# Kernel tuning notes

Measured on AMD Instinct MI355X. Metric: run time of the kernel, lower is better.

## Reference

```python
import jax, jax.numpy as jnp
import numpy as np

DIM = 256
NUM_HEADS = 8
HEAD_DIM = DIM // NUM_HEADS


def _conv1x1(x, W, scale, bias):
    # 1x1 conv (bias=False) + eval-mode BN folded to per-channel scale/shift
    y = jnp.einsum('oc,bchw->bohw', W, x)
    return y * scale[None, :, None, None] + bias[None, :, None, None]


def setup_inputs() -> dict:
    key = jax.random.key(0)
    ks = jax.random.split(key, 16)
    B, H, W = 4, 64, 64
    Hu, Wu = 32, 32
    inp = {
        'x': jax.random.normal(ks[0], (B, DIM, H, W), jnp.float32),
        'upper_feat': jax.random.normal(ks[1], (B, DIM, Hu, Wu), jnp.float32),
        'Wq': jax.random.normal(ks[2], (DIM, DIM), jnp.float32) * 0.02,
        'q_scale': jax.random.uniform(ks[3], (DIM,), jnp.float32, 0.5, 1.5),
        'q_bias': jax.random.normal(ks[4], (DIM,), jnp.float32) * 0.02,
        'Wkv': jax.random.normal(ks[5], (2 * DIM, DIM), jnp.float32) * 0.02,
        'kv_scale': jax.random.uniform(ks[6], (2 * DIM,), jnp.float32, 0.5, 1.5),
        'kv_bias': jax.random.normal(ks[7], (2 * DIM,), jnp.float32) * 0.02,
        'Wpe': jax.random.normal(ks[8], (DIM, 1, 7, 7), jnp.float32) * 0.02,
        'pe_scale': jax.random.uniform(ks[9], (DIM,), jnp.float32, 0.5, 1.5),
        'pe_bias': jax.random.normal(ks[10], (DIM,), jnp.float32) * 0.02,
        'Wproj': jax.random.normal(ks[11], (DIM, DIM), jnp.float32) * 0.02,
        'proj_scale': jax.random.uniform(ks[12], (DIM,), jnp.float32, 0.5, 1.5),
        'proj_bias': jax.random.normal(ks[13], (DIM,), jnp.float32) * 0.02,
    }
    return inp


def reference(x, upper_feat, Wq, q_scale, q_bias, Wkv, kv_scale, kv_bias,
              Wpe, pe_scale, pe_bias, Wproj, proj_scale, proj_bias):
    B, C, H, W = x.shape
    N = H * W
    _, _, Hu, Wu = upper_feat.shape
    Nu = Hu * Wu

    # q branch: 1x1 conv+BN on x -> [B, heads, N, head_dim]
    q = _conv1x1(x, Wq, q_scale, q_bias)
    q = q.reshape(B, NUM_HEADS, HEAD_DIM, N).transpose(0, 1, 3, 2)

    # kv branch on upper (coarser) feature -> [B, heads, Nu, 2*head_dim]
    kv = _conv1x1(upper_feat, Wkv, kv_scale, kv_bias)
    kv = kv.reshape(B, NUM_HEADS, 2 * HEAD_DIM, Nu).transpose(0, 1, 3, 2)
    k, v = kv[..., :HEAD_DIM], kv[..., HEAD_DIM:]

    # cross attention: q over x pixels, k/v over upper pixels
    sim = jnp.einsum('bhnd,bhmd->bhnm', q, k) * (HEAD_DIM ** -0.5)
    attn = jax.nn.softmax(sim, axis=-1)
    ao = jnp.einsum('bhnm,bhmd->bhnd', attn, v)  # [B,h,N,hd]
    ao = ao.transpose(0, 1, 3, 2).reshape(B, C, H, W)

    # positional-encoding branch: depthwise 7x7 conv on v at upper resolution
    v_r = v.transpose(0, 1, 3, 2).reshape(B, C, Hu, Wu)
    v_pe = jax.lax.conv_general_dilated(
        v_r, Wpe, window_strides=(1, 1), padding=((3, 3), (3, 3)),
        feature_group_count=C,
        dimension_numbers=('NCHW', 'OIHW', 'NCHW'))
    v_pe = v_pe * pe_scale[None, :, None, None] + pe_bias[None, :, None, None]
    # bilinear upsample to x resolution (align_corners=False semantics)
    v_pe = jax.image.resize(v_pe, (B, C, H, W), method='bilinear')

    out = ao + v_pe
    return _conv1x1(out, Wproj, proj_scale, proj_bias)
```

## Files before the change

kernel.cpp:

```cpp
#include <hip/hip_runtime.h>
#include <hip/hip_bf16.h>

#define DIM 256
#define NHEADS 8
#define HDIM 32
#define Bq 4
#define Nq 4096
#define Nu 1024

typedef __attribute__((ext_vector_type(8))) short bf16x8;
typedef __attribute__((ext_vector_type(16))) float f32x16;
typedef __attribute__((ext_vector_type(4))) unsigned short us4;

__device__ __forceinline__ ushort f2bf(float x) {
    union { float f; unsigned u; } v; v.f = x;
    unsigned r = v.u + 0x7fffu + ((v.u >> 16) & 1u);
    return (ushort)(r >> 16);
}
__device__ __forceinline__ float bf2f(ushort u) {
    union { unsigned u; float f; } v; v.u = ((unsigned)u) << 16;
    return v.f;
}

__global__ __launch_bounds__(256) void prepro(
    const float* __restrict__ Wq, ushort* __restrict__ Oq,
    const float* __restrict__ Wkv, ushort* __restrict__ Okv,
    const float* __restrict__ Wp, ushort* __restrict__ Oph, ushort* __restrict__ Opl,
    const float* __restrict__ x, ushort* __restrict__ xT,
    const float* __restrict__ upper, ushort* __restrict__ upT)
{
    __shared__ ushort T[64][66];
    const int id = blockIdx.x;
    const int tid = threadIdx.x;

    if (id < 512) {
        int i = id * 256 + tid;
        if (i < 65536) {
            Oq[i] = f2bf(Wq[i]);
            float w = Wp[i];
            ushort h = f2bf(w);
            Oph[i] = h;
            Opl[i] = f2bf(w - bf2f(h));
        }
        Okv[i] = f2bf(Wkv[i]);
        return;
    }

    const float* In; ushort* OutT; int N, n0, c0, b;
    if (id < 1536) {
        int q = id - 512;
        In = x; OutT = xT; N = 4096;
        n0 = (q & 63) * 64; c0 = ((q >> 6) & 3) * 64; b = q >> 8;
    } else {
        int q = id - 1536;
        In = upper; OutT = upT; N = 1024;
        n0 = (q & 15) * 64; c0 = ((q >> 4) & 3) * 64; b = q >> 6;
    }

    const float* Ib = In + ((size_t)b * 256 + c0) * N + n0;
    const int nx = (tid & 15) * 4, cy = tid >> 4;
    #pragma unroll
    for (int p = 0; p < 4; ++p) {
        float4 v = *(const float4*)(Ib + (size_t)(cy + p * 16) * N + nx);
        T[nx + 0][cy + p * 16] = f2bf(v.x);
        T[nx + 1][cy + p * 16] = f2bf(v.y);
        T[nx + 2][cy + p * 16] = f2bf(v.z);
        T[nx + 3][cy + p * 16] = f2bf(v.w);
    }
    __syncthreads();
    ushort* Ob = OutT + ((size_t)b * N + n0) * 256 + c0;
    #pragma unroll
    for (int p = 0; p < 4; ++p) {
        int row = (tid >> 4) + p * 16;
        *(us4*)(Ob + (size_t)row * 256 + (tid & 15) * 4) = *(const us4*)&T[row][(tid & 15) * 4];
    }
}

__global__ __launch_bounds__(256, 4) void qkv_mfma(
    const ushort* __restrict__ Wqb, const ushort* __restrict__ xT,
    const float* __restrict__ q_scale, const float* __restrict__ q_bias, float qmult,
    const ushort* __restrict__ Wkvb, const ushort* __restrict__ upT,
    const float* __restrict__ kv_scale, const float* __restrict__ kv_bias,
    ushort* __restrict__ Qb, ushort* __restrict__ Kb, ushort* __restrict__ Vb)
{
    const int KD = 256;
    const int id = blockIdx.x;
    const int tid = threadIdx.x;
    const int w = tid >> 6, l = tid & 63;
    const int l31 = l & 31, hi = l >> 5;

    const ushort *Wb, *InT, *OutA; const float *scale, *bias;
    int N, n0, o0, b; float mult; bool isT; int bh;
    if (id < 512) {
        int q = id;
        int bx = q & 15, by = (q >> 4) & 7; b = q >> 7;
        N = 4096; n0 = (bx * 4 + w) * 64; o0 = by * 32;
        Wb = Wqb; InT = xT; scale = q_scale; bias = q_bias; mult = qmult;
        isT = true; bh = b * 8 + (o0 >> 5);
        OutA = Qb;
    } else {
        int q = id - 512;
        int bx = q & 3, by = (q >> 2) & 15; b = q >> 6;
        N = 1024; n0 = (bx * 4 + w) * 64; o0 = by * 32;
        Wb = Wkvb; InT = upT; scale = kv_scale; bias = kv_bias; mult = 1.0f;
        isT = ((o0 & 32) == 0); bh = b * 8 + (o0 >> 6);
        OutA = Kb;
    }

    const ushort* Wp = Wb + (size_t)(o0 + l31) * KD + hi * 8;
    const ushort* I0 = InT + ((size_t)b * N + n0 + l31) * KD + hi * 8;
    const ushort* I1 = I0 + (size_t)32 * KD;

    f32x16 acc0 = {}, acc1 = {};
    if (isT) {
        #pragma unroll 8
        for (int kk = 0; kk < KD; kk += 16) {
            bf16x8 wv = *(const bf16x8*)(Wp + kk);
            bf16x8 i0 = *(const bf16x8*)(I0 + kk);
            bf16x8 i1 = *(const bf16x8*)(I1 + kk);
            acc0 = __builtin_amdgcn_mfma_f32_32x32x16_bf16(i0, wv, acc0, 0, 0, 0);
            acc1 = __builtin_amdgcn_mfma_f32_32x32x16_bf16(i1, wv, acc1, 0, 0, 0);
        }
        const float sc = scale[o0 + l31] * mult;
        const float bi = bias[o0 + l31] * mult;
        ushort* Oa = (ushort*)OutA + ((size_t)bh * N) * 32 + l31;
        #pragma unroll
        for (int r = 0; r < 16; ++r) {
            const int dn = (r & 3) + 8 * (r >> 2) + 4 * hi;
            Oa[(size_t)(n0 + dn) * 32]      = f2bf(acc0[r] * sc + bi);
            Oa[(size_t)(n0 + 32 + dn) * 32] = f2bf(acc1[r] * sc + bi);
        }
    } else {
        #pragma unroll 8
        for (int kk = 0; kk < KD; kk += 16) {
            bf16x8 wv = *(const bf16x8*)(Wp + kk);
            bf16x8 i0 = *(const bf16x8*)(I0 + kk);
            bf16x8 i1 = *(const bf16x8*)(I1 + kk);
            acc0 = __builtin_amdgcn_mfma_f32_32x32x16_bf16(wv, i0, acc0, 0, 0, 0);
            acc1 = __builtin_amdgcn_mfma_f32_32x32x16_bf16(wv, i1, acc1, 0, 0, 0);
        }
        ushort* Ob = Vb + (size_t)bh * 32 * N;
        #pragma unroll
        for (int r = 0; r < 16; ++r) {
            const int dr = (r & 3) + 8 * (r >> 2) + 4 * hi;
            const float sc = scale[o0 + dr], bi = bias[o0 + dr];
            Ob[(size_t)dr * N + n0 + l31]      = f2bf(acc0[r] * sc + bi);
            Ob[(size_t)dr * N + n0 + 32 + l31] = f2bf(acc1[r] * sc + bi);
        }
    }
}

__global__ __launch_bounds__(256, 4) void attn_dw(
    const ushort* __restrict__ Qb, const ushort* __restrict__ Kt,
    const ushort* __restrict__ Vb, ushort* __restrict__ ao,
    const float* __restrict__ Wpe, const float* __restrict__ pe_scale,
    const float* __restrict__ pe_bias, ushort* __restrict__ vpe)
{
    __shared__ __align__(16) unsigned char smem[16384];
    const int tid = threadIdx.x;

    if (blockIdx.x < 1024) {
        const int w = tid >> 6, l = tid & 63;
        const int l31 = l & 31, hi = l >> 5;
        const int lid = blockIdx.x;
        const int j = lid >> 3;
        const int bh = (lid & 7) * 4 + (j >> 5);
        const int qbase = (j & 31) * 128 + w * 32;

        unsigned char (*ldsbuf)[8192] = (unsigned char(*)[8192])smem;

        const ushort* Qp = Qb + ((size_t)bh * 4096 + qbase) * 32;
        const unsigned char* Kg = (const unsigned char*)(Kt + (size_t)bh * 1024 * 32);
        const unsigned char* Vg = (const unsigned char*)(Vb + (size_t)bh * 32 * 1024);

        const bf16x8 qb0 = *(const bf16x8*)(Qp + (size_t)l31 * 32 + hi * 8);
        const bf16x8 qb1 = *(const bf16x8*)(Qp + (size_t)l31 * 32 + 16 + hi * 8);

        const int kr = tid >> 2, kc = tid & 3;
        const int vd = tid >> 3, vc = tid & 7;
        const int kwr = (kr * 64 + kc * 16) ^ ((kr & 7) << 4);
        const int vwr = vd * 128 + ((vc ^ (vd & 7)) << 4);

        f32x16 acc = {};
        float l_run = 0.f;

        uint4 kreg = *(const uint4*)(Kg + kr * 64 + kc * 16);
        uint4 vreg = *(const uint4*)(Vg + vd * 2048 + vc * 16);
        *(uint4*)(&ldsbuf[0][kwr]) = kreg;
        *(uint4*)(&ldsbuf[0][4096 + vwr]) = vreg;
        __syncthreads();

        for (int ph = 0; ph < 16; ++ph) {
            const int cur = ph & 1;
            if (ph < 15) {
                const size_t koff = (size_t)(ph + 1) * 4096;
                const int    voff = (ph + 1) * 128;
                kreg = *(const uint4*)(Kg + koff + kr * 64 + kc * 16);
                vreg = *(const uint4*)(Vg + (size_t)vd * 2048 + voff + vc * 16);
            }
            const unsigned char* Kl = &ldsbuf[cur][0];
            const unsigned char* Vl = &ldsbuf[cur][4096];

            #pragma unroll
            for (int s = 0; s < 2; ++s) {
                const int r = s * 32 + l31;
                bf16x8 ka0 = *(const bf16x8*)(Kl + ((r * 64 + hi * 16) ^ ((r & 7) << 4)));
                bf16x8 ka1 = *(const bf16x8*)(Kl + ((r * 64 + 32 + hi * 16) ^ ((r & 7) << 4)));
                bf16x8 va0 = *(const bf16x8*)(Vl + l31 * 128 + (((s * 4 + hi)     ^ (l31 & 7)) << 4));
                bf16x8 va1 = *(const bf16x8*)(Vl + l31 * 128 + (((s * 4 + 2 + hi) ^ (l31 & 7)) << 4));

                f32x16 sv = {};
                sv = __builtin_amdgcn_mfma_f32_32x32x16_bf16(ka0, qb0, sv, 0, 0, 0);
                sv = __builtin_amdgcn_mfma_f32_32x32x16_bf16(ka1, qb1, sv, 0, 0, 0);

                float p[16];
                #pragma unroll
                for (int r2 = 0; r2 < 16; ++r2) p[r2] = __builtin_amdgcn_exp2f(sv[r2]);
                l_run += (((p[0] + p[1]) + (p[2] + p[3])) + ((p[4] + p[5]) + (p[6] + p[7])))
                       + (((p[8] + p[9]) + (p[10] + p[11])) + ((p[12] + p[13]) + (p[14] + p[15])));

                int c[8];
                #pragma unroll
                for (int i = 0; i < 8; ++i)
                    asm("v_cvt_pk_bf16_f32 %0, %1, %2" : "=v"(c[i]) : "v"(p[2 * i]), "v"(p[2 * i + 1]));
                asm("v_permlane32_swap_b32 %0, %1" : "+v"(c[0]), "+v"(c[2]));
                asm("v_permlane32_swap_b32 %0, %1" : "+v"(c[1]), "+v"(c[3]));
                asm("v_permlane32_swap_b32 %0, %1" : "+v"(c[4]), "+v"(c[6]));
                asm("v_permlane32_swap_b32 %0, %1" : "+v"(c[5]), "+v"(c[7]));

                union { int i[4]; bf16x8 v; } b0u, b1u;
                b0u.i[0] = c[0]; b0u.i[1] = c[1]; b0u.i[2] = c[2]; b0u.i[3] = c[3];
                b1u.i[0] = c[4]; b1u.i[1] = c[5]; b1u.i[2] = c[6]; b1u.i[3] = c[7];

                acc = __builtin_amdgcn_mfma_f32_32x32x16_bf16(va0, b0u.v, acc, 0, 0, 0);
                acc = __builtin_amdgcn_mfma_f32_32x32x16_bf16(va1, b1u.v, acc, 0, 0, 0);
            }

            if (ph < 15) {
                const int nxt = cur ^ 1;
                *(uint4*)(&ldsbuf[nxt][kwr]) = kreg;
                *(uint4*)(&ldsbuf[nxt][4096 + vwr]) = vreg;
            }
            __syncthreads();
        }

        l_run += __shfl_xor(l_run, 32);
        float inv = 1.0f / l_run;

        ushort* aob = ao + ((size_t)(bh >> 3) * 256 + (bh & 7) * 32) * 4096 + qbase + l31;
        #pragma unroll
        for (int r = 0; r < 16; ++r) {
            const int d = (r & 3) + 8 * (r >> 2) + 4 * hi;
            aob[(size_t)d * 4096] = f2bf(acc[r] * inv);
        }
    } else {
        const int bc = blockIdx.x - 1024;
        const int b = bc >> 8, c = bc & 255;
        const ushort* vp = Vb + ((size_t)(b * 8 + (c >> 5)) * 32 + (c & 31)) * 1024;

        float* t   = (float*)smem;
        float* v32 = (float*)(smem + 5776);
        float* wl  = (float*)(smem + 9872);

        for (int i = tid; i < 38 * 38; i += 256) {
            int yy = i / 38 - 3, xx = i % 38 - 3;
            t[i] = (yy >= 0 && yy < 32 && xx >= 0 && xx < 32) ? bf2f(vp[yy * 32 + xx]) : 0.f;
        }
        if (tid < 49) wl[tid] = Wpe[(size_t)c * 49 + tid];
        __syncthreads();

        const float sc = pe_scale[c], bi = pe_bias[c];
        for (int i = tid; i < 1024; i += 256) {
            int y = i >> 5, x = i & 31;
            float s = 0.f;
            #pragma unroll
            for (int ky = 0; ky < 7; ++ky)
                #pragma unroll
                for (int kx = 0; kx < 7; ++kx)
                    s += t[(y + ky) * 38 + x + kx] * wl[ky * 7 + kx];
            v32[i] = s * sc + bi;
        }
        __syncthreads();

        ushort* op = vpe + (size_t)bc * 4096;
        #pragma unroll
        for (int p = 0; p < 16; ++p) {
            int idx = p * 256 + tid;
            int x = idx & 63, y = idx >> 6;
            float cx = x * 0.5f - 0.25f;
            float cy = y * 0.5f - 0.25f;
            int x0 = (x - 1) >> 1, y0 = (y - 1) >> 1;
            float fx = cx - x0, fy = cy - y0;
            int x0c = max(x0, 0), x1c = min(x0 + 1, 31);
            int y0c = max(y0, 0), y1c = min(y0 + 1, 31);
            float v00 = v32[y0c * 32 + x0c], v01 = v32[y0c * 32 + x1c];
            float v10 = v32[y1c * 32 + x0c], v11 = v32[y1c * 32 + x1c];
            float val = (1.f - fy) * ((1.f - fx) * v00 + fx * v01)
                      + fy * ((1.f - fx) * v10 + fx * v11);
            op[idx] = f2bf(val);
        }
    }
}

__global__ __launch_bounds__(256) void prep(
    const ushort* __restrict__ ao, const ushort* __restrict__ vpe,
    ushort* __restrict__ AT)
{
    __shared__ ushort T[64][66];
    const int n0 = blockIdx.x * 64, c0 = blockIdx.y * 64, b = blockIdx.z;
    const int tid = threadIdx.x;
    const ushort* ab = ao  + ((size_t)b * 256 + c0) * 4096 + n0;
    const ushort* vb = vpe + ((size_t)b * 256 + c0) * 4096 + n0;
    const int nx = (tid & 15) * 4, cy = tid >> 4;
    #pragma unroll
    for (int p = 0; p < 4; ++p) {
        const int c = cy + p * 16;
        us4 a = *(const us4*)(ab + (size_t)c * 4096 + nx);
        us4 v = *(const us4*)(vb + (size_t)c * 4096 + nx);
        T[nx + 0][c] = f2bf(bf2f(a.x) + bf2f(v.x));
        T[nx + 1][c] = f2bf(bf2f(a.y) + bf2f(v.y));
        T[nx + 2][c] = f2bf(bf2f(a.z) + bf2f(v.z));
        T[nx + 3][c] = f2bf(bf2f(a.w) + bf2f(v.w));
    }
    __syncthreads();
    ushort* Ob = AT + ((size_t)b * 4096 + n0) * 256 + c0;
    #pragma unroll
    for (int p = 0; p < 4; ++p) {
        int row = (tid >> 4) + p * 16;
        *(us4*)(Ob + (size_t)row * 256 + (tid & 15) * 4) = *(const us4*)&T[row][(tid & 15) * 4];
    }
}

__global__ __launch_bounds__(256, 2) void proj_mfma(
    const ushort* __restrict__ Whi, const ushort* __restrict__ Wlo,
    const ushort* __restrict__ A,
    const float* __restrict__ scale, const float* __restrict__ bias,
    float* __restrict__ Out)
{
    const int KD = 256;
    const int tid = threadIdx.x;
    const int w = tid >> 6, l = tid & 63;
    const int l31 = l & 31, hi = l >> 5;
    const int b = blockIdx.z;
    const int n0 = (blockIdx.x * 4 + w) * 64;
    const int o0 = blockIdx.y * 32;

    const ushort* wh  = Whi + (size_t)(o0 + l31) * KD + hi * 8;
    const ushort* wlp = Wlo + (size_t)(o0 + l31) * KD + hi * 8;
    const ushort* a0  = A + ((size_t)b * 4096 + n0 + l31) * KD + hi * 8;
    const ushort* a1  = a0 + (size_t)32 * KD;

    f32x16 acc0 = {}, acc1 = {};
    #pragma unroll 4
    for (int kk = 0; kk < KD; kk += 16) {
        bf16x8 awh = *(const bf16x8*)(wh + kk);
        bf16x8 awl = *(const bf16x8*)(wlp + kk);
        bf16x8 av0 = *(const bf16x8*)(a0 + kk);
        bf16x8 av1 = *(const bf16x8*)(a1 + kk);
        acc0 = __builtin_amdgcn_mfma_f32_32x32x16_bf16(awh, av0, acc0, 0, 0, 0);
        acc1 = __builtin_amdgcn_mfma_f32_32x32x16_bf16(awh, av1, acc1, 0, 0, 0);
        acc0 = __builtin_amdgcn_mfma_f32_32x32x16_bf16(awl, av0, acc0, 0, 0, 0);
        acc1 = __builtin_amdgcn_mfma_f32_32x32x16_bf16(awl, av1, acc1, 0, 0, 0);
    }

    float* Ob = Out + (size_t)b * 256 * 4096;
    #pragma unroll
    for (int r = 0; r < 16; ++r) {
        const int o = o0 + (r & 3) + 8 * (r >> 2) + 4 * hi;
        const float sc = scale[o], bi = bias[o];
        Ob[(size_t)o * 4096 + n0 + l31]      = acc0[r] * sc + bi;
        Ob[(size_t)o * 4096 + n0 + 32 + l31] = acc1[r] * sc + bi;
    }
}

extern "C" void kernel_launch(void* const* d_in, const int* in_sizes, int n_in,
                              void* d_out, int out_size, void* d_ws, size_t ws_size,
                              hipStream_t stream)
{
    const float* x        = (const float*)d_in[0];
    const float* upper    = (const float*)d_in[1];
    const float* Wq       = (const float*)d_in[2];
    const float* q_scale  = (const float*)d_in[3];
    const float* q_bias   = (const float*)d_in[4];
    const float* Wkv      = (const float*)d_in[5];
    const float* kv_scale = (const float*)d_in[6];
    const float* kv_bias  = (const float*)d_in[7];
    const float* Wpe      = (const float*)d_in[8];
    const float* pe_scale = (const float*)d_in[9];
    const float* pe_bias  = (const float*)d_in[10];
    const float* Wproj    = (const float*)d_in[11];
    const float* proj_scale = (const float*)d_in[12];
    const float* proj_bias  = (const float*)d_in[13];
    float* out = (float*)d_out;

    ushort* Qb   = (ushort*)d_ws;
    ushort* Kb   = Qb + (size_t)32 * 4096 * 32;
    ushort* Vb   = Kb + (size_t)32 * 1024 * 32;
    ushort* ao   = Vb + (size_t)32 * 1024 * 32;
    ushort* AT   = ao + (size_t)Bq * DIM * Nq;
    ushort* Wqb  = AT + (size_t)Bq * Nq * DIM;
    ushort* Wkvb = Wqb + 256 * 256;
    ushort* Wph  = Wkvb + 512 * 256;
    ushort* Wpl  = Wph + 256 * 256;
    ushort* xT   = ao;
    ushort* upT  = AT;
    ushort* vpe  = (ushort*)out;

    const float qmult = 0.17677669529663687f * 1.4426950408889634f;

    prepro<<<dim3(1792), 256, 0, stream>>>(Wq, Wqb, Wkv, Wkvb, Wproj, Wph, Wpl,
                                           x, xT, upper, upT);

    qkv_mfma<<<dim3(768), 256, 0, stream>>>(Wqb, xT, q_scale, q_bias, qmult,
                                            Wkvb, upT, kv_scale, kv_bias,
                                            Qb, Kb, Vb);

    attn_dw<<<dim3(2048), 256, 0, stream>>>(Qb, Kb, Vb, ao,
                                            Wpe, pe_scale, pe_bias, vpe);

    prep<<<dim3(64, 4, 4), 256, 0, stream>>>(ao, vpe, AT);

    proj_mfma<<<dim3(16, 8, 4), 256, 0, stream>>>(Wph, Wpl, AT,
                                                  proj_scale, proj_bias, out);
}
```

Measured before the change: 90.13 us.

## Fuse residual add and transpose into projection GEMM via swizzled LDS tile

Removes the separate prep kernel, which summed ao and vpe and wrote a transposed bf16 buffer. Each proj_mfma block now loads a 64-pixel by 256-channel tile of both inputs, adds them, packs to bf16 and stores it transposed into XOR-swizzled shared memory before the MFMA loop reads it. The tiling also changes: each block covers 128 output channels, which lets the staged activations be reused across more weight rows, and vpe gets its own workspace buffer instead of aliasing the output. The cost is 32KB of LDS per block, which may limit occupancy, and each of the two o-blocks per tile re-reads and re-adds the same inputs.

```diff
diff --git a/kernel.cpp b/kernel.cpp
--- a/kernel.cpp
+++ b/kernel.cpp
@@ -302,74 +302,96 @@
     }
 }
 
-__global__ __launch_bounds__(256) void prep(
-    const ushort* __restrict__ ao, const ushort* __restrict__ vpe,
-    ushort* __restrict__ AT)
-{
-    __shared__ ushort T[64][66];
-    const int n0 = blockIdx.x * 64, c0 = blockIdx.y * 64, b = blockIdx.z;
-    const int tid = threadIdx.x;
-    const ushort* ab = ao  + ((size_t)b * 256 + c0) * 4096 + n0;
-    const ushort* vb = vpe + ((size_t)b * 256 + c0) * 4096 + n0;
-    const int nx = (tid & 15) * 4, cy = tid >> 4;
-    #pragma unroll
-    for (int p = 0; p < 4; ++p) {
-        const int c = cy + p * 16;
-        us4 a = *(const us4*)(ab + (size_t)c * 4096 + nx);
-        us4 v = *(const us4*)(vb + (size_t)c * 4096 + nx);
-        T[nx + 0][c] = f2bf(bf2f(a.x) + bf2f(v.x));
-        T[nx + 1][c] = f2bf(bf2f(a.y) + bf2f(v.y));
-        T[nx + 2][c] = f2bf(bf2f(a.z) + bf2f(v.z));
-        T[nx + 3][c] = f2bf(bf2f(a.w) + bf2f(v.w));
-    }
-    __syncthreads();
-    ushort* Ob = AT + ((size_t)b * 4096 + n0) * 256 + c0;
-    #pragma unroll
-    for (int p = 0; p < 4; ++p) {
-        int row = (tid >> 4) + p * 16;
-        *(us4*)(Ob + (size_t)row * 256 + (tid & 15) * 4) = *(const us4*)&T[row][(tid & 15) * 4];
-    }
-}
-
 __global__ __launch_bounds__(256, 2) void proj_mfma(
     const ushort* __restrict__ Whi, const ushort* __restrict__ Wlo,
-    const ushort* __restrict__ A,
+    const ushort* __restrict__ ao, const ushort* __restrict__ vpe,
     const float* __restrict__ scale, const float* __restrict__ bias,
     float* __restrict__ Out)
 {
-    const int KD = 256;
+    __shared__ __align__(16) ushort S[64 * 256];
     const int tid = threadIdx.x;
+    const int b  = blockIdx.z;
+    const int n0 = blockIdx.x * 64;
+    const int o0 = blockIdx.y * 128;
+
+    {
+        const int n8 = (tid & 7) * 8;
+        const int c8 = (tid >> 3) * 8;
+        const ushort* ap = ao  + ((size_t)b * 256 + c8) * 4096 + n0 + n8;
+        const ushort* vp = vpe + ((size_t)b * 256 + c8) * 4096 + n0 + n8;
+        unsigned ow[8][4];
+        #pragma unroll
+        for (int rp = 0; rp < 4; ++rp) {
+            uint4 a0 = *(const uint4*)(ap + (size_t)(2 * rp) * 4096);
+            uint4 a1 = *(const uint4*)(ap + (size_t)(2 * rp + 1) * 4096);
+            uint4 v0 = *(const uint4*)(vp + (size_t)(2 * rp) * 4096);
+            uint4 v1 = *(const uint4*)(vp + (size_t)(2 * rp + 1) * 4096);
+            const unsigned* a0u = (const unsigned*)&a0;
+            const unsigned* a1u = (const unsigned*)&a1;
+            const unsigned* v0u = (const unsigned*)&v0;
+            const unsigned* v1u = (const unsigned*)&v1;
+            #pragma unroll
+            for (int q = 0; q < 4; ++q) {
+                float s0lo = __uint_as_float(a0u[q] << 16)
+                           + __uint_as_float(v0u[q] << 16);
+                float s0hi = __uint_as_float(a0u[q] & 0xffff0000u)
+                           + __uint_as_float(v0u[q] & 0xffff0000u);
+                float s1lo = __uint_as_float(a1u[q] << 16)
+                           + __uint_as_float(v1u[q] << 16);
+                float s1hi = __uint_as_float(a1u[q] & 0xffff0000u)
+                           + __uint_as_float(v1u[q] & 0xffff0000u);
+                unsigned plo, phi;
+                asm("v_cvt_pk_bf16_f32 %0, %1, %2" : "=v"(plo) : "v"(s0lo), "v"(s1lo));
+                asm("v_cvt_pk_bf16_f32 %0, %1, %2" : "=v"(phi) : "v"(s0hi), "v"(s1hi));
+                ow[2 * q][rp]     = plo;
+                ow[2 * q + 1][rp] = phi;
+            }
+        }
+        #pragma unroll
+        for (int j = 0; j < 8; ++j) {
+            const int n = n8 + j;
+            const int slot = (((c8 >> 3) ^ (n & 15)) & 31);
+            *(uint4*)(&S[n * 256 + (slot << 3)]) = *(const uint4*)&ow[j][0];
+        }
+    }
+    __syncthreads();
+
     const int w = tid >> 6, l = tid & 63;
     const int l31 = l & 31, hi = l >> 5;
-    const int b = blockIdx.z;
-    const int n0 = (blockIdx.x * 4 + w) * 64;
-    const int o0 = blockIdx.y * 32;
-
-    const ushort* wh  = Whi + (size_t)(o0 + l31) * KD + hi * 8;
-    const ushort* wlp = Wlo + (size_t)(o0 + l31) * KD + hi * 8;
-    const ushort* a0  = A + ((size_t)b * 4096 + n0 + l31) * KD + hi * 8;
-    const ushort* a1  = a0 + (size_t)32 * KD;
+    const int wo = w >> 1, wn = w & 1;
+    const int ob = o0 + wo * 64;
+
+    const ushort* wh0 = Whi + (size_t)(ob + l31) * 256 + hi * 8;
+    const ushort* wh1 = wh0 + (size_t)32 * 256;
+    const ushort* wl0 = Wlo + (size_t)(ob + l31) * 256 + hi * 8;
+    const ushort* wl1 = wl0 + (size_t)32 * 256;
+
+    const int nloc = wn * 32 + l31;
+    const ushort* Srow = &S[nloc * 256];
+    const int nsw = nloc & 15;
 
     f32x16 acc0 = {}, acc1 = {};
     #pragma unroll 4
-    for (int kk = 0; kk < KD; kk += 16) {
-        bf16x8 awh = *(const bf16x8*)(wh + kk);
-        bf16x8 awl = *(const bf16x8*)(wlp + kk);
-        bf16x8 av0 = *(const bf16x8*)(a0 + kk);
-        bf16x8 av1 = *(const bf16x8*)(a1 + kk);
-        acc0 = __builtin_amdgcn_mfma_f32_32x32x16_bf16(awh, av0, acc0, 0, 0, 0);
-        acc1 = __builtin_amdgcn_mfma_f32_32x32x16_bf16(awh, av1, acc1, 0, 0, 0);
-        acc0 = __builtin_amdgcn_mfma_f32_32x32x16_bf16(awl, av0, acc0, 0, 0, 0);
-        acc1 = __builtin_amdgcn_mfma_f32_32x32x16_bf16(awl, av1, acc1, 0, 0, 0);
-    }
-
-    float* Ob = Out + (size_t)b * 256 * 4096;
+    for (int kk = 0; kk < 256; kk += 16) {
+        const int slot = (((kk >> 3) + hi) ^ nsw) & 31;
+        bf16x8 av = *(const bf16x8*)(Srow + (slot << 3));
+        bf16x8 h0 = *(const bf16x8*)(wh0 + kk);
+        bf16x8 h1 = *(const bf16x8*)(wh1 + kk);
+        bf16x8 g0 = *(const bf16x8*)(wl0 + kk);
+        bf16x8 g1 = *(const bf16x8*)(wl1 + kk);
+        acc0 = __builtin_amdgcn_mfma_f32_32x32x16_bf16(h0, av, acc0, 0, 0, 0);
+        acc1 = __builtin_amdgcn_mfma_f32_32x32x16_bf16(h1, av, acc1, 0, 0, 0);
+        acc0 = __builtin_amdgcn_mfma_f32_32x32x16_bf16(g0, av, acc0, 0, 0, 0);
+        acc1 = __builtin_amdgcn_mfma_f32_32x32x16_bf16(g1, av, acc1, 0, 0, 0);
+    }
+
+    float* Ob = Out + (size_t)b * 256 * 4096 + n0 + wn * 32 + l31;
     #pragma unroll
     for (int r = 0; r < 16; ++r) {
-        const int o = o0 + (r & 3) + 8 * (r >> 2) + 4 * hi;
-        const float sc = scale[o], bi = bias[o];
-        Ob[(size_t)o * 4096 + n0 + l31]      = acc0[r] * sc + bi;
-        Ob[(size_t)o * 4096 + n0 + 32 + l31] = acc1[r] * sc + bi;
+        const int dr = (r & 3) + 8 * (r >> 2) + 4 * hi;
+        const int oA = ob + dr, oB = ob + 32 + dr;
+        Ob[(size_t)oA * 4096] = acc0[r] * scale[oA] + bias[oA];
+        Ob[(size_t)oB * 4096] = acc1[r] * scale[oB] + bias[oB];
     }
 }
 
@@ -397,14 +419,13 @@
     ushort* Kb   = Qb + (size_t)32 * 4096 * 32;
     ushort* Vb   = Kb + (size_t)32 * 1024 * 32;
     ushort* ao   = Vb + (size_t)32 * 1024 * 32;
-    ushort* AT   = ao + (size_t)Bq * DIM * Nq;
-    ushort* Wqb  = AT + (size_t)Bq * Nq * DIM;
+    ushort* vpe  = ao + (size_t)Bq * DIM * Nq;
+    ushort* Wqb  = vpe + (size_t)Bq * DIM * Nq;
     ushort* Wkvb = Wqb + 256 * 256;
     ushort* Wph  = Wkvb + 512 * 256;
     ushort* Wpl  = Wph + 256 * 256;
     ushort* xT   = ao;
-    ushort* upT  = AT;
-    ushort* vpe  = (ushort*)out;
+    ushort* upT  = vpe;
 
     const float qmult = 0.17677669529663687f * 1.4426950408889634f;
 
@@ -418,8 +439,6 @@
     attn_dw<<<dim3(2048), 256, 0, stream>>>(Qb, Kb, Vb, ao,
                                             Wpe, pe_scale, pe_bias, vpe);
 
-    prep<<<dim3(64, 4, 4), 256, 0, stream>>>(ao, vpe, AT);
-
-    proj_mfma<<<dim3(16, 8, 4), 256, 0, stream>>>(Wph, Wpl, AT,
+    proj_mfma<<<dim3(64, 2, 4), 256, 0, stream>>>(Wph, Wpl, ao, vpe,
                                                   proj_scale, proj_bias, out);
 }
```

Result: no change. 88.80 us (-1.5%).
